# Kernel tuning notes

Hardware: AMD Instinct MI355X
Metric: run time of the kernel (lower is better)

## Reference

```python
import jax, jax.numpy as jnp
import numpy as np

N_NODES = 50000
N_EDGES = 600000
F_IN = 57
HID = 128
NEG_SLOPE = 0.2  # PyG GATConv default leaky_relu slope


def setup_inputs() -> dict:
    key = jax.random.key(0)
    ks = jax.random.split(key, 10)
    s = lambda k, shape, fan: jax.random.normal(k, shape, jnp.float32) / np.float32(np.sqrt(fan))
    x = jax.random.normal(ks[0], (N_NODES, F_IN), jnp.float32)
    edge_index = jax.random.randint(ks[1], (2, N_EDGES), 0, N_NODES)
    return {
        "x": x,
        "edge_index": edge_index,
        # layer1: GATConv(57 -> 128, heads=1)
        "W_gat": s(ks[2], (F_IN, HID), F_IN),
        "a_src": s(ks[3], (HID,), HID),
        "a_dst": s(ks[4], (HID,), HID),
        "b_gat": jnp.zeros((HID,), jnp.float32),
        # layer2: SAGEConv(128 -> 128, aggr='mean'): lin_l (with bias) on aggregated, lin_r (no bias) on self
        "W_l": s(ks[5], (HID, HID), HID),
        "b_l": jnp.zeros((HID,), jnp.float32),
        "W_r": s(ks[6], (HID, HID), HID),
        # layer3: Linear(128 -> 1)
        "W_out": s(ks[7], (HID, 1), HID),
        "b_out": jnp.zeros((1,), jnp.float32),
    }


def _gat_conv(x, src, dst, W, a_s, a_d, b, n):
    # PyG GATConv (heads=1): adds self-loops, attention softmax over incoming edges per dst node.
    loop = jnp.arange(n)
    src = jnp.concatenate([src, loop])
    dst = jnp.concatenate([dst, loop])
    h = x @ W                                   # [N, H]
    logit = jax.nn.leaky_relu((h @ a_s)[src] + (h @ a_d)[dst], NEG_SLOPE)  # [E+N]
    lmax = jax.lax.stop_gradient(jax.ops.segment_max(logit, dst, num_segments=n))
    ex = jnp.exp(logit - lmax[dst])
    denom = jax.ops.segment_sum(ex, dst, num_segments=n)
    alpha = ex / denom[dst]
    out = jax.ops.segment_sum(alpha[:, None] * h[src], dst, num_segments=n)  # [N, H]
    return out + b


def _sage_conv_mean(x, src, dst, W_l, b_l, W_r, n):
    # PyG SAGEConv: out = lin_l(mean_{j->i} x_j) + lin_r(x_i); no self-loops.
    msum = jax.ops.segment_sum(x[src], dst, num_segments=n)          # [N, H]
    cnt = jax.ops.segment_sum(jnp.ones_like(src, jnp.float32), dst, num_segments=n)
    mean = msum / jnp.maximum(cnt, 1.0)[:, None]
    return mean @ W_l + b_l + x @ W_r


def reference(x, edge_index, W_gat, a_src, a_dst, b_gat, W_l, b_l, W_r, W_out, b_out):
    n = x.shape[0]
    src, dst = edge_index[0], edge_index[1]
    h = jax.nn.relu(_gat_conv(x, src, dst, W_gat, a_src, a_dst, b_gat, n))
    h = jax.nn.relu(_sage_conv_mean(h, src, dst, W_l, b_l, W_r, n))
    return jax.nn.sigmoid(h @ W_out + b_out)  # [N, 1]
```

## Files before the change

kernel.cpp:

```cpp
#include <hip/hip_runtime.h>

#define NN 50000
#define NE 600000
#define F_IN 57
#define HID 128
#define NEG 0.2f
#define NB_SCAN ((NN + 255) / 256)

#define GIN_NODES 64
#define NB_GIN ((NN + GIN_NODES - 1) / GIN_NODES)
#define XST 68
#define NB_PACK 16
#define NZERO_INT4 ((2 * NN + 4 + 3) / 4)
#define NB_ZERO ((NZERO_INT4 + 255) / 256)

#define DN_NODES 64
#define NB_DENSE ((NN + DN_NODES - 1) / DN_NODES)

typedef unsigned short bf16_t;
typedef __attribute__((ext_vector_type(8))) short bf16x8;
typedef __attribute__((ext_vector_type(4))) float f32x4;

__device__ __forceinline__ float leaky(float v) { return v >= 0.f ? v : NEG * v; }
__device__ __forceinline__ float bf2f(bf16_t u) { return __uint_as_float(((unsigned)u) << 16); }
__device__ __forceinline__ bf16_t f2bf(float f) {
    unsigned u = __float_as_uint(f);
    return (bf16_t)((u + 0x7FFFu + ((u >> 16) & 1u)) >> 16);
}

__global__ __launch_bounds__(256) void k_front(
    const float* __restrict__ x, const float* __restrict__ Wg,
    const float* __restrict__ a_s, const float* __restrict__ a_d,
    const float* __restrict__ Wl, const float* __restrict__ Wr,
    bf16_t* __restrict__ h, float* __restrict__ hs, float* __restrict__ hd,
    bf16_t* __restrict__ Bp, int* __restrict__ zbase) {
    int tid = threadIdx.x;

    if (blockIdx.x >= NB_GIN + NB_PACK) {
        int idx4 = (blockIdx.x - NB_GIN - NB_PACK) * 256 + tid;
        if (idx4 < NZERO_INT4) *(int4*)(zbase + idx4 * 4) = (int4){0, 0, 0, 0};
        return;
    }
    if (blockIdx.x >= NB_GIN) {
        int idx = (blockIdx.x - NB_GIN) * 256 + tid;
        if (idx >= 8 * 8 * 64) return;
        int lane = idx & 63;
        int kb = (idx >> 6) & 7;
        int nt = idx >> 9;
        int col = nt * 16 + (lane & 15);
        int kbase = kb * 32 + (lane >> 4) * 8;
        bf16_t v[8];
#pragma unroll
        for (int j = 0; j < 8; ++j) {
            int k = kbase + j;
            float w = (k < HID) ? Wl[k * HID + col] : Wr[(k - HID) * HID + col];
            v[j] = f2bf(w);
        }
        ushort4* o = (ushort4*)(Bp + (size_t)idx * 8);
        ushort4 lo, hi;
        lo.x = v[0]; lo.y = v[1]; lo.z = v[2]; lo.w = v[3];
        hi.x = v[4]; hi.y = v[5]; hi.z = v[6]; hi.w = v[7];
        o[0] = lo; o[1] = hi;
        return;
    }

    __shared__ float WgS[F_IN * HID];
    __shared__ float xsT[F_IN][XST];
    int node0 = blockIdx.x * GIN_NODES;
    {
        const float4* g = (const float4*)Wg;
        float4* s = (float4*)WgS;
        for (int i = tid; i < F_IN * HID / 4; i += 256) s[i] = g[i];
    }
    for (int i = tid; i < GIN_NODES * F_IN; i += 256) {
        int n = i / F_IN;
        int k = i - n * F_IN;
        int gn = node0 + n;
        if (gn >= NN) gn = NN - 1;
        xsT[k][n] = x[gn * F_IN + k];
    }
    __syncthreads();

    int fq = tid & 31, nq = tid >> 5;
    int f0 = fq * 4, nb = nq * 8;
    float acc[8][4];
#pragma unroll
    for (int i = 0; i < 8; ++i)
#pragma unroll
        for (int j = 0; j < 4; ++j) acc[i][j] = 0.f;

    for (int k = 0; k < F_IN; ++k) {
        float4 w = *(const float4*)&WgS[k * HID + f0];
        float4 xa = *(const float4*)&xsT[k][nb];
        float4 xb = *(const float4*)&xsT[k][nb + 4];
        float xv[8] = {xa.x, xa.y, xa.z, xa.w, xb.x, xb.y, xb.z, xb.w};
        float wv[4] = {w.x, w.y, w.z, w.w};
#pragma unroll
        for (int i = 0; i < 8; ++i)
#pragma unroll
            for (int j = 0; j < 4; ++j)
                acc[i][j] = fmaf(xv[i], wv[j], acc[i][j]);
    }

    float4 as4 = *(const float4*)(a_s + f0);
    float4 ad4 = *(const float4*)(a_d + f0);
    float ps[8], pd[8];
#pragma unroll
    for (int i = 0; i < 8; ++i) {
        int gn = node0 + nb + i;
        if (gn < NN) {
            ushort4 hv;
            hv.x = f2bf(acc[i][0]); hv.y = f2bf(acc[i][1]);
            hv.z = f2bf(acc[i][2]); hv.w = f2bf(acc[i][3]);
            *(ushort4*)(h + (size_t)gn * HID + f0) = hv;
        }
        ps[i] = acc[i][0] * as4.x + acc[i][1] * as4.y + acc[i][2] * as4.z + acc[i][3] * as4.w;
        pd[i] = acc[i][0] * ad4.x + acc[i][1] * ad4.y + acc[i][2] * ad4.z + acc[i][3] * ad4.w;
    }
#pragma unroll
    for (int off = 16; off > 0; off >>= 1) {
#pragma unroll
        for (int i = 0; i < 8; ++i) {
            ps[i] += __shfl_xor(ps[i], off);
            pd[i] += __shfl_xor(pd[i], off);
        }
    }
    if (fq == 0) {
#pragma unroll
        for (int i = 0; i < 8; ++i) {
            int gn = node0 + nb + i;
            if (gn < NN) { hs[gn] = ps[i]; hd[gn] = pd[i]; }
        }
    }
}

__global__ void k_hist(const int* __restrict__ dst, int* __restrict__ deg) {
    int e = blockIdx.x * blockDim.x + threadIdx.x;
    if (e < NE) atomicAdd(&deg[dst[e]], 1);
}

__global__ void k_scan(const int* __restrict__ deg, int* __restrict__ rptr,
                       int* __restrict__ bsum, int* __restrict__ bpre,
                       int* __restrict__ done) {
    int t = threadIdx.x;
    int tile = blockIdx.x;
    int i = tile * 256 + t;
    int v = (i < NN) ? deg[i] : 0;
    __shared__ int s[256];
    __shared__ int islast;
    s[t] = v;
    __syncthreads();
    for (int off = 1; off < 256; off <<= 1) {
        int xv = (t >= off) ? s[t - off] : 0;
        __syncthreads();
        s[t] += xv;
        __syncthreads();
    }
    if (i < NN) rptr[i] = s[t] - v;
    if (t == 255) bsum[tile] = s[255];
    __threadfence();
    if (t == 0) islast = (atomicAdd(done, 1) == NB_SCAN - 1);
    __syncthreads();
    if (!islast) return;
    int b = (t < NB_SCAN) ? atomicAdd(&bsum[t], 0) : 0;
    __syncthreads();
    s[t] = b;
    __syncthreads();
    for (int off = 1; off < 256; off <<= 1) {
        int xv = (t >= off) ? s[t - off] : 0;
        __syncthreads();
        s[t] += xv;
        __syncthreads();
    }
    if (t < NB_SCAN) bpre[t] = s[t] - b;
}

__global__ void k_fill(const int* __restrict__ src, const int* __restrict__ dst,
                       const int* __restrict__ rptr, const int* __restrict__ bpre,
                       int* __restrict__ fillcnt, int* __restrict__ esrc) {
    int e = blockIdx.x * blockDim.x + threadIdx.x;
    if (e >= NE) return;
    int d = dst[e];
    int pos = rptr[d] + bpre[d >> 8] + atomicAdd(&fillcnt[d], 1);
    esrc[pos] = src[e];
}

__global__ __launch_bounds__(256) void k_gat_agg(
    const int* __restrict__ rptr, const int* __restrict__ bpre,
    const int* __restrict__ deg, const int* __restrict__ esrc,
    const float* __restrict__ hs, const float* __restrict__ hd,
    const bf16_t* __restrict__ h, const float* __restrict__ bg,
    bf16_t* __restrict__ h1) {
    int tid = threadIdx.x;
    int row = blockIdx.x * 4 + (tid >> 6);
    if (row >= NN) return;
    int lane = tid & 63;
    int slot = lane >> 4;
    int f8 = lane & 15;

    int start = rptr[row] + bpre[row >> 8];
    int dn = deg[row];
    int end = start + dn;
    float hdr = hd[row];
    float wself = __expf(leaky(hs[row] + hdr));

    float a[8];
#pragma unroll
    for (int j = 0; j < 8; ++j) a[j] = 0.f;
    float denL = 0.f;

    if (slot == 0) {
        bf16x8 r = *(const bf16x8*)(h + (size_t)row * HID + f8 * 8);
#pragma unroll
        for (int j = 0; j < 8; ++j) a[j] = wself * bf2f((bf16_t)r[j]);
    }

    int e = start;
    for (; e + 8 <= end; e += 8) {
        int s0 = esrc[e + slot];
        int s1 = esrc[e + 4 + slot];
        float w0 = __expf(leaky(hs[s0] + hdr));
        float w1 = __expf(leaky(hs[s1] + hdr));
        bf16x8 r0 = *(const bf16x8*)(h + (size_t)s0 * HID + f8 * 8);
        bf16x8 r1 = *(const bf16x8*)(h + (size_t)s1 * HID + f8 * 8);
        denL += w0 + w1;
#pragma unroll
        for (int j = 0; j < 8; ++j) {
            a[j] = fmaf(w0, bf2f((bf16_t)r0[j]), a[j]);
            a[j] = fmaf(w1, bf2f((bf16_t)r1[j]), a[j]);
        }
    }
    for (; e < end; e += 4) {
        int i = e + slot;
        bool act = i < end;
        int sn = esrc[act ? i : end - 1];
        float w = act ? __expf(leaky(hs[sn] + hdr)) : 0.f;
        bf16x8 r = *(const bf16x8*)(h + (size_t)sn * HID + f8 * 8);
        denL += w;
#pragma unroll
        for (int j = 0; j < 8; ++j) a[j] = fmaf(w, bf2f((bf16_t)r[j]), a[j]);
    }

#pragma unroll
    for (int j = 0; j < 8; ++j) {
        a[j] += __shfl_xor(a[j], 16);
        a[j] += __shfl_xor(a[j], 32);
    }
    denL += __shfl_xor(denL, 16);
    denL += __shfl_xor(denL, 32);
    float inv = 1.f / (wself + denL);

    if (lane < 16) {
        float4 b0 = *(const float4*)(bg + lane * 8);
        float4 b1 = *(const float4*)(bg + lane * 8 + 4);
        float bb[8] = {b0.x, b0.y, b0.z, b0.w, b1.x, b1.y, b1.z, b1.w};
        bf16x8 o;
#pragma unroll
        for (int j = 0; j < 8; ++j) {
            float v = a[j] * inv + bb[j];
            o[j] = (short)f2bf(v > 0.f ? v : 0.f);
        }
        *(bf16x8*)(h1 + (size_t)row * HID + lane * 8) = o;
    }
}

__global__ __launch_bounds__(256) void k_sage_gather(
    const int* __restrict__ rptr, const int* __restrict__ bpre,
    const int* __restrict__ deg, const int* __restrict__ esrc,
    const bf16_t* __restrict__ h1, bf16_t* __restrict__ mean) {
    int tid = threadIdx.x;
    int row = blockIdx.x * 4 + (tid >> 6);
    if (row >= NN) return;
    int lane = tid & 63;
    int slot = lane >> 4;
    int f8 = lane & 15;

    int start = rptr[row] + bpre[row >> 8];
    int dn = deg[row];
    int end = start + dn;

    float a[8];
#pragma unroll
    for (int j = 0; j < 8; ++j) a[j] = 0.f;

    int e = start;
    for (; e + 8 <= end; e += 8) {
        int s0 = esrc[e + slot];
        int s1 = esrc[e + 4 + slot];
        bf16x8 r0 = *(const bf16x8*)(h1 + (size_t)s0 * HID + f8 * 8);
        bf16x8 r1 = *(const bf16x8*)(h1 + (size_t)s1 * HID + f8 * 8);
#pragma unroll
        for (int j = 0; j < 8; ++j)
            a[j] += bf2f((bf16_t)r0[j]) + bf2f((bf16_t)r1[j]);
    }
    for (; e < end; e += 4) {
        int i = e + slot;
        bool act = i < end;
        int sn = esrc[act ? i : end - 1];
        bf16x8 r = *(const bf16x8*)(h1 + (size_t)sn * HID + f8 * 8);
        float w = act ? 1.f : 0.f;
#pragma unroll
        for (int j = 0; j < 8; ++j) a[j] = fmaf(w, bf2f((bf16_t)r[j]), a[j]);
    }

#pragma unroll
    for (int j = 0; j < 8; ++j) {
        a[j] += __shfl_xor(a[j], 16);
        a[j] += __shfl_xor(a[j], 32);
    }
    if (lane < 16) {
        float inv = 1.f / (float)(dn > 0 ? dn : 1);
        bf16x8 o;
#pragma unroll
        for (int j = 0; j < 8; ++j) o[j] = (short)f2bf(a[j] * inv);
        *(bf16x8*)(mean + (size_t)row * HID + lane * 8) = o;
    }
}

__global__ __launch_bounds__(256) void k_dense_mfma(
    const bf16_t* __restrict__ mean, const bf16_t* __restrict__ h1,
    const bf16_t* __restrict__ Bp, const float* __restrict__ bl,
    const float* __restrict__ Wout, const float* __restrict__ bout,
    float* __restrict__ out) {
    int tid = threadIdx.x;
    int lane = tid & 63;
    int wv = tid >> 6;
    int node0 = blockIdx.x * DN_NODES + wv * 16;
    int arow = lane & 15;
    int kg = lane >> 4;
    int gn = node0 + arow;
    if (gn >= NN) gn = NN - 1;
    const bf16_t* mrow = mean + (size_t)gn * HID;
    const bf16_t* srow = h1 + (size_t)gn * HID;
    const bf16x8* bp = (const bf16x8*)Bp;

    f32x4 acc[8];
#pragma unroll
    for (int n = 0; n < 8; ++n) acc[n] = (f32x4){0.f, 0.f, 0.f, 0.f};

#pragma unroll
    for (int kb = 0; kb < 8; ++kb) {
        int k0 = kb * 32 + kg * 8;
        bf16x8 a = (kb < 4) ? *(const bf16x8*)(mrow + k0)
                            : *(const bf16x8*)(srow + (k0 - HID));
#pragma unroll
        for (int n = 0; n < 8; ++n) {
            bf16x8 b = bp[((n * 8 + kb) << 6) + lane];
            acc[n] = __builtin_amdgcn_mfma_f32_16x16x32_bf16(a, b, acc[n], 0, 0, 0);
        }
    }

    float pr[4] = {0.f, 0.f, 0.f, 0.f};
#pragma unroll
    for (int n = 0; n < 8; ++n) {
        int f = n * 16 + arow;
        float b = bl[f];
        float wo = Wout[f];
#pragma unroll
        for (int r = 0; r < 4; ++r) {
            float v = fmaxf(acc[n][r] + b, 0.f);
            pr[r] = fmaf(v, wo, pr[r]);
        }
    }
#pragma unroll
    for (int off = 8; off > 0; off >>= 1) {
#pragma unroll
        for (int r = 0; r < 4; ++r) pr[r] += __shfl_xor(pr[r], off);
    }
    if (arow == 0) {
        float bo = bout[0];
#pragma unroll
        for (int r = 0; r < 4; ++r) {
            int gno = node0 + kg * 4 + r;
            if (gno < NN) out[gno] = 1.f / (1.f + __expf(-(pr[r] + bo)));
        }
    }
}

extern "C" void kernel_launch(void* const* d_in, const int* in_sizes, int n_in,
                              void* d_out, int out_size, void* d_ws, size_t ws_size,
                              hipStream_t stream) {
    const float* x    = (const float*)d_in[0];
    const int*   ei   = (const int*)d_in[1];
    const float* Wg   = (const float*)d_in[2];
    const float* a_s  = (const float*)d_in[3];
    const float* a_d  = (const float*)d_in[4];
    const float* bg   = (const float*)d_in[5];
    const float* Wl   = (const float*)d_in[6];
    const float* bl   = (const float*)d_in[7];
    const float* Wr   = (const float*)d_in[8];
    const float* Wout = (const float*)d_in[9];
    const float* bout = (const float*)d_in[10];
    float* out = (float*)d_out;

    const int* src = ei;
    const int* dst = ei + NE;

    bf16_t* h    = (bf16_t*)d_ws;
    bf16_t* h1   = h + (size_t)NN * HID;
    bf16_t* mean = h1 + (size_t)NN * HID;
    bf16_t* Bp   = mean + (size_t)NN * HID;
    float* hs = (float*)(Bp + 8 * 8 * 64 * 8);
    float* hd = hs + NN;
    int* deg     = (int*)(hd + NN);
    int* fillcnt = deg + NN;
    int* done    = fillcnt + NN;
    int* rptr    = done + 4;
    int* bsum    = rptr + NN;
    int* bpre    = bsum + 256;
    int* esrc    = bpre + 256;

    k_front<<<NB_GIN + NB_PACK + NB_ZERO, 256, 0, stream>>>(
        x, Wg, a_s, a_d, Wl, Wr, h, hs, hd, Bp, deg);

    k_hist<<<(NE + 255) / 256, 256, 0, stream>>>(dst, deg);
    k_scan<<<NB_SCAN, 256, 0, stream>>>(deg, rptr, bsum, bpre, done);
    k_fill<<<(NE + 255) / 256, 256, 0, stream>>>(src, dst, rptr, bpre, fillcnt, esrc);

    k_gat_agg<<<(NN + 3) / 4, 256, 0, stream>>>(rptr, bpre, deg, esrc, hs, hd, h, bg, h1);
    k_sage_gather<<<(NN + 3) / 4, 256, 0, stream>>>(rptr, bpre, deg, esrc, h1, mean);
    k_dense_mfma<<<NB_DENSE, 256, 0, stream>>>(mean, h1, Bp, bl, Wout, bout, out);
}
```

Baseline: 175.0 us.

## Fuse SAGE mean gather with MFMA dense layer via shared memory

Merges the SAGE neighbor-mean gather and the MFMA dense/output kernel into one kernel. Each block gathers 16 nodes' means and self rows into LDS, then four waves each compute two 16-column output tiles and reduce the output dot product through shared memory. This removes the global round-trip of the mean buffer (50000x128 bf16) and one kernel launch. In exchange each block does more serial gather work per wave, and each block reloads the full packed weight matrix for only 16 nodes. NB_SD assumes NN is divisible by 16.

```diff
diff --git a/kernel.cpp b/kernel.cpp
--- a/kernel.cpp
+++ b/kernel.cpp
@@ -14,8 +14,8 @@
 #define NZERO_INT4 ((2 * NN + 4 + 3) / 4)
 #define NB_ZERO ((NZERO_INT4 + 255) / 256)
 
-#define DN_NODES 64
-#define NB_DENSE ((NN + DN_NODES - 1) / DN_NODES)
+#define SD_NODES 16
+#define NB_SD (NN / SD_NODES)
 
 typedef unsigned short bf16_t;
 typedef __attribute__((ext_vector_type(8))) short bf16x8;
@@ -264,102 +264,102 @@
     }
 }
 
-__global__ __launch_bounds__(256) void k_sage_gather(
+__global__ __launch_bounds__(256) void k_sage_dense(
     const int* __restrict__ rptr, const int* __restrict__ bpre,
     const int* __restrict__ deg, const int* __restrict__ esrc,
-    const bf16_t* __restrict__ h1, bf16_t* __restrict__ mean) {
+    const bf16_t* __restrict__ h1, const bf16_t* __restrict__ Bp,
+    const float* __restrict__ bl, const float* __restrict__ Wout,
+    const float* __restrict__ bout, float* __restrict__ out) {
+    __shared__ __align__(16) bf16_t meanS[SD_NODES][136];
+    __shared__ __align__(16) bf16_t selfS[SD_NODES][136];
+    __shared__ float prS[4][SD_NODES];
     int tid = threadIdx.x;
-    int row = blockIdx.x * 4 + (tid >> 6);
-    if (row >= NN) return;
+    int wv = tid >> 6;
     int lane = tid & 63;
     int slot = lane >> 4;
     int f8 = lane & 15;
-
-    int start = rptr[row] + bpre[row >> 8];
-    int dn = deg[row];
-    int end = start + dn;
-
-    float a[8];
-#pragma unroll
-    for (int j = 0; j < 8; ++j) a[j] = 0.f;
-
-    int e = start;
-    for (; e + 8 <= end; e += 8) {
-        int s0 = esrc[e + slot];
-        int s1 = esrc[e + 4 + slot];
-        bf16x8 r0 = *(const bf16x8*)(h1 + (size_t)s0 * HID + f8 * 8);
-        bf16x8 r1 = *(const bf16x8*)(h1 + (size_t)s1 * HID + f8 * 8);
-#pragma unroll
-        for (int j = 0; j < 8; ++j)
-            a[j] += bf2f((bf16_t)r0[j]) + bf2f((bf16_t)r1[j]);
-    }
-    for (; e < end; e += 4) {
-        int i = e + slot;
-        bool act = i < end;
-        int sn = esrc[act ? i : end - 1];
-        bf16x8 r = *(const bf16x8*)(h1 + (size_t)sn * HID + f8 * 8);
-        float w = act ? 1.f : 0.f;
-#pragma unroll
-        for (int j = 0; j < 8; ++j) a[j] = fmaf(w, bf2f((bf16_t)r[j]), a[j]);
-    }
-
-#pragma unroll
-    for (int j = 0; j < 8; ++j) {
-        a[j] += __shfl_xor(a[j], 16);
-        a[j] += __shfl_xor(a[j], 32);
-    }
-    if (lane < 16) {
-        float inv = 1.f / (float)(dn > 0 ? dn : 1);
-        bf16x8 o;
-#pragma unroll
-        for (int j = 0; j < 8; ++j) o[j] = (short)f2bf(a[j] * inv);
-        *(bf16x8*)(mean + (size_t)row * HID + lane * 8) = o;
-    }
-}
-
-__global__ __launch_bounds__(256) void k_dense_mfma(
-    const bf16_t* __restrict__ mean, const bf16_t* __restrict__ h1,
-    const bf16_t* __restrict__ Bp, const float* __restrict__ bl,
-    const float* __restrict__ Wout, const float* __restrict__ bout,
-    float* __restrict__ out) {
-    int tid = threadIdx.x;
-    int lane = tid & 63;
-    int wv = tid >> 6;
-    int node0 = blockIdx.x * DN_NODES + wv * 16;
+    int node0 = blockIdx.x * SD_NODES;
+
+#pragma unroll
+    for (int i = 0; i < 4; ++i) {
+        int ln = wv * 4 + i;
+        int row = node0 + ln;
+        int start = rptr[row] + bpre[row >> 8];
+        int dn = deg[row];
+        int end = start + dn;
+
+        bf16x8 selfr;
+        if (slot == 1) selfr = *(const bf16x8*)(h1 + (size_t)row * HID + f8 * 8);
+
+        float a[8];
+#pragma unroll
+        for (int j = 0; j < 8; ++j) a[j] = 0.f;
+
+        int e = start;
+        for (; e + 8 <= end; e += 8) {
+            int s0 = esrc[e + slot];
+            int s1 = esrc[e + 4 + slot];
+            bf16x8 r0 = *(const bf16x8*)(h1 + (size_t)s0 * HID + f8 * 8);
+            bf16x8 r1 = *(const bf16x8*)(h1 + (size_t)s1 * HID + f8 * 8);
+#pragma unroll
+            for (int j = 0; j < 8; ++j)
+                a[j] += bf2f((bf16_t)r0[j]) + bf2f((bf16_t)r1[j]);
+        }
+        for (; e < end; e += 4) {
+            int ie = e + slot;
+            bool act = ie < end;
+            int sn = esrc[act ? ie : end - 1];
+            bf16x8 r = *(const bf16x8*)(h1 + (size_t)sn * HID + f8 * 8);
+            float w = act ? 1.f : 0.f;
+#pragma unroll
+            for (int j = 0; j < 8; ++j) a[j] = fmaf(w, bf2f((bf16_t)r[j]), a[j]);
+        }
+
+#pragma unroll
+        for (int j = 0; j < 8; ++j) {
+            a[j] += __shfl_xor(a[j], 16);
+            a[j] += __shfl_xor(a[j], 32);
+        }
+        if (lane < 16) {
+            float inv = 1.f / (float)(dn > 0 ? dn : 1);
+            bf16x8 o;
+#pragma unroll
+            for (int j = 0; j < 8; ++j) o[j] = (short)f2bf(a[j] * inv);
+            *(bf16x8*)&meanS[ln][lane * 8] = o;
+        }
+        if (slot == 1) *(bf16x8*)&selfS[ln][f8 * 8] = selfr;
+    }
+    __syncthreads();
+
     int arow = lane & 15;
     int kg = lane >> 4;
-    int gn = node0 + arow;
-    if (gn >= NN) gn = NN - 1;
-    const bf16_t* mrow = mean + (size_t)gn * HID;
-    const bf16_t* srow = h1 + (size_t)gn * HID;
     const bf16x8* bp = (const bf16x8*)Bp;
-
-    f32x4 acc[8];
-#pragma unroll
-    for (int n = 0; n < 8; ++n) acc[n] = (f32x4){0.f, 0.f, 0.f, 0.f};
+    f32x4 acc0 = (f32x4){0.f, 0.f, 0.f, 0.f};
+    f32x4 acc1 = (f32x4){0.f, 0.f, 0.f, 0.f};
+    int n0 = wv * 2;
 
 #pragma unroll
     for (int kb = 0; kb < 8; ++kb) {
         int k0 = kb * 32 + kg * 8;
-        bf16x8 a = (kb < 4) ? *(const bf16x8*)(mrow + k0)
-                            : *(const bf16x8*)(srow + (k0 - HID));
-#pragma unroll
-        for (int n = 0; n < 8; ++n) {
-            bf16x8 b = bp[((n * 8 + kb) << 6) + lane];
-            acc[n] = __builtin_amdgcn_mfma_f32_16x16x32_bf16(a, b, acc[n], 0, 0, 0);
-        }
+        bf16x8 a = (kb < 4) ? *(const bf16x8*)&meanS[arow][k0]
+                            : *(const bf16x8*)&selfS[arow][k0 - HID];
+        bf16x8 b0 = bp[(((n0 + 0) * 8 + kb) << 6) + lane];
+        bf16x8 b1 = bp[(((n0 + 1) * 8 + kb) << 6) + lane];
+        acc0 = __builtin_amdgcn_mfma_f32_16x16x32_bf16(a, b0, acc0, 0, 0, 0);
+        acc1 = __builtin_amdgcn_mfma_f32_16x16x32_bf16(a, b1, acc1, 0, 0, 0);
     }
 
     float pr[4] = {0.f, 0.f, 0.f, 0.f};
-#pragma unroll
-    for (int n = 0; n < 8; ++n) {
-        int f = n * 16 + arow;
-        float b = bl[f];
-        float wo = Wout[f];
+    {
+        int f0 = (n0 + 0) * 16 + arow;
+        int f1 = (n0 + 1) * 16 + arow;
+        float bl0 = bl[f0], bl1 = bl[f1];
+        float wo0 = Wout[f0], wo1 = Wout[f1];
 #pragma unroll
         for (int r = 0; r < 4; ++r) {
-            float v = fmaxf(acc[n][r] + b, 0.f);
-            pr[r] = fmaf(v, wo, pr[r]);
+            float v0 = fmaxf(acc0[r] + bl0, 0.f);
+            float v1 = fmaxf(acc1[r] + bl1, 0.f);
+            pr[r] = fmaf(v0, wo0, fmaf(v1, wo1, pr[r]));
         }
     }
 #pragma unroll
@@ -368,12 +368,13 @@
         for (int r = 0; r < 4; ++r) pr[r] += __shfl_xor(pr[r], off);
     }
     if (arow == 0) {
-        float bo = bout[0];
-#pragma unroll
-        for (int r = 0; r < 4; ++r) {
-            int gno = node0 + kg * 4 + r;
-            if (gno < NN) out[gno] = 1.f / (1.f + __expf(-(pr[r] + bo)));
-        }
+#pragma unroll
+        for (int r = 0; r < 4; ++r) prS[wv][kg * 4 + r] = pr[r];
+    }
+    __syncthreads();
+    if (tid < SD_NODES) {
+        float z = prS[0][tid] + prS[1][tid] + prS[2][tid] + prS[3][tid] + bout[0];
+        out[node0 + tid] = 1.f / (1.f + __expf(-z));
     }
 }
 
@@ -398,8 +399,7 @@
 
     bf16_t* h    = (bf16_t*)d_ws;
     bf16_t* h1   = h + (size_t)NN * HID;
-    bf16_t* mean = h1 + (size_t)NN * HID;
-    bf16_t* Bp   = mean + (size_t)NN * HID;
+    bf16_t* Bp   = h1 + (size_t)NN * HID;
     float* hs = (float*)(Bp + 8 * 8 * 64 * 8);
     float* hd = hs + NN;
     int* deg     = (int*)(hd + NN);
@@ -418,6 +418,5 @@
     k_fill<<<(NE + 255) / 256, 256, 0, stream>>>(src, dst, rptr, bpre, fillcnt, esrc);
 
     k_gat_agg<<<(NN + 3) / 4, 256, 0, stream>>>(rptr, bpre, deg, esrc, hs, hd, h, bg, h1);
-    k_sage_gather<<<(NN + 3) / 4, 256, 0, stream>>>(rptr, bpre, deg, esrc, h1, mean);
-    k_dense_mfma<<<NB_DENSE, 256, 0, stream>>>(mean, h1, Bp, bl, Wout, bout, out);
-}
+    k_sage_dense<<<NB_SD, 256, 0, stream>>>(rptr, bpre, deg, esrc, h1, Bp, bl, Wout, bout, out);
+}
```

Measured after the change: 170.2 us. 1.03x faster.
